# Performance work log

Measured on AMD Instinct MI355X. Metric: run time of the kernel, lower is better.

Reference implementation:

```python
import jax, jax.numpy as jnp
import numpy as np

EMBED_DIM = 1024
N_HEAD = 16
BLOCK_SIZE = 2048
B, T = 4, 2048


def setup_inputs() -> dict:
    key = jax.random.key(0)
    kx, kw, kb = jax.random.split(key, 3)
    x = jax.random.normal(kx, (B, T, EMBED_DIM), dtype=jnp.float32)
    # nn.Linear(embed_dim, 3*embed_dim): weight [3C, C], bias [3C]
    bound = 1.0 / np.sqrt(EMBED_DIM)
    W_qkv = jax.random.uniform(kw, (3 * EMBED_DIM, EMBED_DIM), dtype=jnp.float32, minval=-bound, maxval=bound)
    b_qkv = jax.random.uniform(kb, (3 * EMBED_DIM,), dtype=jnp.float32, minval=-bound, maxval=bound)
    return {"x": x, "W_qkv": W_qkv, "b_qkv": b_qkv}


def reference(x, W_qkv, b_qkv):
    Bsz, Tlen, C = x.shape
    H = N_HEAD
    hd = C // H
    qkv = x @ W_qkv.T + b_qkv  # [B, T, 3C]
    q, k, v = jnp.split(qkv, 3, axis=2)
    # [B, H, T, hd]
    q = q.reshape(Bsz, Tlen, H, hd).transpose(0, 2, 1, 3)
    k = k.reshape(Bsz, Tlen, H, hd).transpose(0, 2, 1, 3)
    v = v.reshape(Bsz, Tlen, H, hd).transpose(0, 2, 1, 3)
    att = jnp.einsum('bhqd,bhkd->bhqk', q, k) / np.sqrt(hd).astype(np.float32)
    causal = jnp.tril(jnp.ones((Tlen, Tlen), dtype=bool))
    att = jnp.where(causal[None, None, :, :], att, -jnp.inf)
    att = jax.nn.softmax(att, axis=-1)
    out = jnp.einsum('bhqk,bhkd->bhqd', att, v)  # [B, H, T, hd]
    y = out.transpose(0, 2, 1, 3).reshape(Bsz, Tlen, C)
    return y
```

## Files before the change

### kernel.cpp

```cpp
#include <hip/hip_runtime.h>


typedef unsigned short u16;
typedef short bf16x8 __attribute__((ext_vector_type(8)));
typedef float f32x4 __attribute__((ext_vector_type(4)));
typedef float f32x16 __attribute__((ext_vector_type(16)));

__device__ __forceinline__ float exp2f_hw(float x) {
  return __builtin_amdgcn_exp2f(x);
}

__device__ __forceinline__ u16 f2b(float f) {
  union { float f; unsigned u; } x; x.f = f;
  unsigned r = x.u + 0x7FFFu + ((x.u >> 16) & 1u);
  return (u16)(r >> 16);
}

__device__ __forceinline__ unsigned cvtpk(float lo, float hi_) {
  unsigned r;
  asm("v_cvt_pk_bf16_f32 %0, %1, %2" : "=v"(r) : "v"(lo), "v"(hi_));
  return r;
}

__device__ __forceinline__ void gload16(const void* g, void* l) {
  __builtin_amdgcn_global_load_lds(
      (const __attribute__((address_space(1))) unsigned*)g,
      (__attribute__((address_space(3))) unsigned*)l, 16, 0, 0);
}

__device__ __forceinline__ void packP(f32x16 st, bf16x8& pa0, bf16x8& pa1) {
#pragma unroll
  for (int r = 0; r < 16; ++r) st[r] = exp2f_hw(fminf(st[r], 80.f));
  {
    unsigned x0 = cvtpk(st[0], st[1]),  y0 = cvtpk(st[4], st[5]);
    unsigned x1 = cvtpk(st[2], st[3]),  y1 = cvtpk(st[6], st[7]);
    auto s0 = __builtin_amdgcn_permlane32_swap(x0, y0, false, false);
    auto s1 = __builtin_amdgcn_permlane32_swap(x1, y1, false, false);
    union { unsigned w[4]; bf16x8 v; } u;
    u.w[0] = s0[0]; u.w[1] = s1[0]; u.w[2] = s0[1]; u.w[3] = s1[1];
    pa0 = u.v;
  }
  {
    unsigned x0 = cvtpk(st[8], st[9]),   y0 = cvtpk(st[12], st[13]);
    unsigned x1 = cvtpk(st[10], st[11]), y1 = cvtpk(st[14], st[15]);
    auto s0 = __builtin_amdgcn_permlane32_swap(x0, y0, false, false);
    auto s1 = __builtin_amdgcn_permlane32_swap(x1, y1, false, false);
    union { unsigned w[4]; bf16x8 v; } u;
    u.w[0] = s0[0]; u.w[1] = s1[0]; u.w[2] = s0[1]; u.w[3] = s1[1];
    pa1 = u.v;
  }
}

__global__ void cvt_bf16(const float* __restrict__ src, u16* __restrict__ dst, int n4) {
  int i = blockIdx.x * blockDim.x + threadIdx.x;
  const int stride = gridDim.x * blockDim.x;
  for (; i < n4; i += stride) {
    float4 v = ((const float4*)src)[i];
    ushort4 o;
    o.x = f2b(v.x); o.y = f2b(v.y); o.z = f2b(v.z); o.w = f2b(v.w);
    ((ushort4*)dst)[i] = o;
  }
}

__global__ __launch_bounds__(256) void qkv_gemm(
    const u16* __restrict__ Xb, const u16* __restrict__ Wb,
    const float* __restrict__ bias,
    u16* __restrict__ qw, u16* __restrict__ kw, u16* __restrict__ vw) {
  __shared__ u16 LDSbuf[2][16384];
  const int tid  = threadIdx.x;
  const int lane = tid & 63;
  const int wave = tid >> 6;
  const int ln = lane & 15, hi = lane >> 4;
  const int wr = wave >> 1, wc = wave & 1;
  const int m0 = blockIdx.y * 128;
  const int n0 = blockIdx.x * 128;
  const bool vblk = (n0 >= 2048);

  const int srow = tid >> 2;
  const int scol = (tid & 3) * 8;

  f32x4 zero = {0.f, 0.f, 0.f, 0.f};
  f32x4 acc[4][4];
#pragma unroll
  for (int i = 0; i < 4; ++i)
#pragma unroll
    for (int j = 0; j < 4; ++j) acc[i][j] = zero;

  const u16* Xb0 = Xb + (size_t)(m0 + srow) * 1024 + scol;
  const u16* Xb1 = Xb + (size_t)(m0 + 64 + srow) * 1024 + scol;
  const u16* Wb0 = Wb + (size_t)(n0 + srow) * 1024 + scol;
  const u16* Wb1 = Wb + (size_t)(n0 + 64 + srow) * 1024 + scol;

  auto STAGE = [&](int cur, int k0) {
    char* As = (char*)&LDSbuf[cur][0];
    char* Bs = (char*)&LDSbuf[cur][8192];
    gload16(Xb0 + k0,      As + tid * 16);
    gload16(Xb1 + k0,      As + 4096 + tid * 16);
    gload16(Xb0 + k0 + 32, As + 8192 + tid * 16);
    gload16(Xb1 + k0 + 32, As + 12288 + tid * 16);
    gload16(Wb0 + k0,      Bs + tid * 16);
    gload16(Wb1 + k0,      Bs + 4096 + tid * 16);
    gload16(Wb0 + k0 + 32, Bs + 8192 + tid * 16);
    gload16(Wb1 + k0 + 32, Bs + 12288 + tid * 16);
  };

  auto COMPUTE = [&](int cur) {
    const u16* As = &LDSbuf[cur][0];
    const u16* Bs = &LDSbuf[cur][8192];
#pragma unroll
    for (int hf = 0; hf < 2; ++hf) {
      const u16* Ah = As + hf * 4096;
      const u16* Bh = Bs + hf * 4096;
      bf16x8 af[4], bfv[4];
#pragma unroll
      for (int i = 0; i < 4; ++i)
        af[i] = *(const bf16x8*)&Ah[(wr * 64 + i * 16 + ln) * 32 + hi * 8];
#pragma unroll
      for (int j = 0; j < 4; ++j)
        bfv[j] = *(const bf16x8*)&Bh[(wc * 64 + j * 16 + ln) * 32 + hi * 8];
      if (vblk) {
#pragma unroll
        for (int i = 0; i < 4; ++i)
#pragma unroll
          for (int j = 0; j < 4; ++j)
            acc[i][j] = __builtin_amdgcn_mfma_f32_16x16x32_bf16(bfv[j], af[i], acc[i][j], 0, 0, 0);
      } else {
#pragma unroll
        for (int i = 0; i < 4; ++i)
#pragma unroll
          for (int j = 0; j < 4; ++j)
            acc[i][j] = __builtin_amdgcn_mfma_f32_16x16x32_bf16(af[i], bfv[j], acc[i][j], 0, 0, 0);
      }
    }
  };

  STAGE(0, 0);
  __syncthreads();
  int cur = 0;
#pragma unroll 1
  for (int t = 0; t < 15; ++t) {
    STAGE(cur ^ 1, (t + 1) * 64);
    COMPUTE(cur);
    __syncthreads();
    cur ^= 1;
  }
  COMPUTE(cur);

  const int which = n0 >> 10;
  const int h = ((n0 & 1023) >> 6) + wc;
  const size_t bh = (size_t)((m0 >> 11) * 16 + h);
  const int tloc = (m0 & 2047) + wr * 64;

  if (which == 2) {
    u16* ob = vw + bh * 131072;
#pragma unroll
    for (int j = 0; j < 4; ++j) {
      float bv[4];
#pragma unroll
      for (int r = 0; r < 4; ++r) bv[r] = bias[n0 + wc * 64 + j * 16 + hi * 4 + r];
#pragma unroll
      for (int i = 0; i < 4; ++i) {
        u16* p = ob + (((tloc >> 4) + i) * 64 + j * 16 + hi * 4) * 16 + ln;
#pragma unroll
        for (int r = 0; r < 4; ++r)
          p[r * 16] = f2b(acc[i][j][r] + bv[r]);
      }
    }
  } else {
    u16* ob = (which == 0 ? qw : kw) + bh * 131072;
    const float qs = (which == 0) ? 0.1803368801111244f : 1.0f;
    const int t5 = tloc >> 5;
#pragma unroll
    for (int j = 0; j < 4; ++j) {
      const float bv = bias[n0 + wc * 64 + j * 16 + ln];
#pragma unroll
      for (int i = 0; i < 4; ++i) {
        u16* p = ob + ((t5 + (i >> 1)) * 4 + j) * 512 + ((i & 1) * 16 + hi * 4) * 16 + ln;
#pragma unroll
        for (int r = 0; r < 4; ++r)
          p[r * 16] = f2b((acc[i][j][r] + bv) * qs);
      }
    }
  }
}

__global__ __launch_bounds__(128) void attn(
    const u16* __restrict__ qw, const u16* __restrict__ kw,
    const u16* __restrict__ vw, float* __restrict__ y) {
  __shared__ float accXA[2][16][64];
  __shared__ float lXA[2][16][64];
  __shared__ float accXB[2][16][64];
  __shared__ float lXB[2][16][64];

  const int lane = threadIdx.x & 63;
  const int p    = threadIdx.x >> 6;
  const int l31 = lane & 31;
  const int hi  = lane >> 5;
  const int laneoff = l31 * 16 + hi * 8;

  const int bid = blockIdx.x;
  const int xcd = bid & 7;
  const int rest = bid >> 3;
  const int pr  = rest & 15;
  const int bh  = xcd + 8 * (rest >> 4);
  const int bb  = bh >> 4, h = bh & 15;

  const u16* qb = qw + (size_t)bh * 131072;
  const u16* kb = kw + (size_t)bh * 131072;
  const u16* vb = vw + (size_t)bh * 131072;
  float* yb = y + (size_t)bb * 2048 * 1024 + (size_t)h * 64;

  bf16x8 onesf;
#pragma unroll
  for (int j = 0; j < 8; ++j) onesf[j] = (short)0x3F80;

#pragma unroll 1
  for (int phase = 0; phase < 2; ++phase) {
    const int s  = phase ? (31 - pr) : pr;
    const int q0 = s * 64;
    const int cA = 2 * s, cB = 2 * s + 1;
    const int jtE = cB;

    bf16x8 qfA[4], qfB[4];
#pragma unroll
    for (int sb = 0; sb < 4; ++sb) {
      qfA[sb] = *(const bf16x8*)&qb[(cA * 4 + sb) * 512 + laneoff];
      qfB[sb] = *(const bf16x8*)&qb[(cB * 4 + sb) * 512 + laneoff];
    }

    f32x16 accA0, accA1, acclA, accB0, accB1, acclB;
#pragma unroll
    for (int r = 0; r < 16; ++r) {
      accA0[r] = 0.f; accA1[r] = 0.f; acclA[r] = 0.f;
      accB0[r] = 0.f; accB1[r] = 0.f; acclB[r] = 0.f;
    }

    bf16x8 kf[4];
#pragma unroll
    for (int sb = 0; sb < 4; ++sb)
      kf[sb] = *(const bf16x8*)&kb[(p * 4 + sb) * 512 + laneoff];

#pragma unroll 1
    for (int jt = p; jt <= jtE; jt += 2) {
      bf16x8 vf[4];
      vf[0] = *(const bf16x8*)&vb[((jt * 2 + 0) * 64 +  0 + l31) * 16 + hi * 8];
      vf[1] = *(const bf16x8*)&vb[((jt * 2 + 0) * 64 + 32 + l31) * 16 + hi * 8];
      vf[2] = *(const bf16x8*)&vb[((jt * 2 + 1) * 64 +  0 + l31) * 16 + hi * 8];
      vf[3] = *(const bf16x8*)&vb[((jt * 2 + 1) * 64 + 32 + l31) * 16 + hi * 8];

      f32x16 stA, stB;
#pragma unroll
      for (int r = 0; r < 16; ++r) { stA[r] = 0.f; stB[r] = 0.f; }
#pragma unroll
      for (int sb = 0; sb < 4; ++sb) {
        stA = __builtin_amdgcn_mfma_f32_32x32x16_bf16(kf[sb], qfA[sb], stA, 0, 0, 0);
        stB = __builtin_amdgcn_mfma_f32_32x32x16_bf16(kf[sb], qfB[sb], stB, 0, 0, 0);
      }
      if (jt + 2 <= jtE) {
#pragma unroll
        for (int sb = 0; sb < 4; ++sb)
          kf[sb] = *(const bf16x8*)&kb[((jt + 2) * 4 + sb) * 512 + laneoff];
      }

      if (jt == cA) {
#pragma unroll
        for (int r = 0; r < 16; ++r) {
          const int crow = (r & 3) + 8 * (r >> 2) + 4 * hi;
          if (crow > l31) stA[r] = -1e30f;
        }
      }
      if (jt == cB) {
#pragma unroll
        for (int r = 0; r < 16; ++r) {
          const int crow = (r & 3) + 8 * (r >> 2) + 4 * hi;
          stA[r] = -1e30f;
          if (crow > l31) stB[r] = -1e30f;
        }
      }

      bf16x8 pa0, pa1;
      packP(stA, pa0, pa1);
      accA0 = __builtin_amdgcn_mfma_f32_32x32x16_bf16(pa0, vf[0], accA0, 0, 0, 0);
      accA1 = __builtin_amdgcn_mfma_f32_32x32x16_bf16(pa0, vf[1], accA1, 0, 0, 0);
      acclA = __builtin_amdgcn_mfma_f32_32x32x16_bf16(pa0, onesf, acclA, 0, 0, 0);
      accA0 = __builtin_amdgcn_mfma_f32_32x32x16_bf16(pa1, vf[2], accA0, 0, 0, 0);
      accA1 = __builtin_amdgcn_mfma_f32_32x32x16_bf16(pa1, vf[3], accA1, 0, 0, 0);
      acclA = __builtin_amdgcn_mfma_f32_32x32x16_bf16(pa1, onesf, acclA, 0, 0, 0);

      packP(stB, pa0, pa1);
      accB0 = __builtin_amdgcn_mfma_f32_32x32x16_bf16(pa0, vf[0], accB0, 0, 0, 0);
      accB1 = __builtin_amdgcn_mfma_f32_32x32x16_bf16(pa0, vf[1], accB1, 0, 0, 0);
      acclB = __builtin_amdgcn_mfma_f32_32x32x16_bf16(pa0, onesf, acclB, 0, 0, 0);
      accB0 = __builtin_amdgcn_mfma_f32_32x32x16_bf16(pa1, vf[2], accB0, 0, 0, 0);
      accB1 = __builtin_amdgcn_mfma_f32_32x32x16_bf16(pa1, vf[3], accB1, 0, 0, 0);
      acclB = __builtin_amdgcn_mfma_f32_32x32x16_bf16(pa1, onesf, acclB, 0, 0, 0);
    }

    __syncthreads();
    if (p == 0) {
#pragma unroll
      for (int r = 0; r < 16; ++r) {
        accXA[0][r][lane] = accA1[r]; lXA[0][r][lane] = acclA[r];
        accXB[0][r][lane] = accB1[r]; lXB[0][r][lane] = acclB[r];
      }
    } else {
#pragma unroll
      for (int r = 0; r < 16; ++r) {
        accXA[1][r][lane] = accA0[r]; lXA[1][r][lane] = acclA[r];
        accXB[1][r][lane] = accB0[r]; lXB[1][r][lane] = acclB[r];
      }
    }
    __syncthreads();

#pragma unroll
    for (int r = 0; r < 16; ++r) {
      const int crow = (r & 3) + 8 * (r >> 2) + 4 * hi;
      const float ownA = (p == 0) ? accA0[r] : accA1[r];
      const float othA = accXA[p ^ 1][r][lane];
      const float invA = 1.0f / (acclA[r] + lXA[p ^ 1][r][lane]);
      yb[(size_t)(q0 + crow) * 1024 + p * 32 + l31] = (ownA + othA) * invA;

      const float ownB = (p == 0) ? accB0[r] : accB1[r];
      const float othB = accXB[p ^ 1][r][lane];
      const float invB = 1.0f / (acclB[r] + lXB[p ^ 1][r][lane]);
      yb[(size_t)(q0 + 32 + crow) * 1024 + p * 32 + l31] = (ownB + othB) * invB;
    }
  }
}

extern "C" void kernel_launch(void* const* d_in, const int* in_sizes, int n_in,
                              void* d_out, int out_size, void* d_ws, size_t ws_size,
                              hipStream_t stream) {
  const float* x    = (const float*)d_in[0];
  const float* W    = (const float*)d_in[1];
  const float* bias = (const float*)d_in[2];
  float* y = (float*)d_out;

  char* ws = (char*)d_ws;
  u16* xb = (u16*)(ws);
  u16* Wb = (u16*)(ws + 16777216);
  u16* qw = (u16*)(ws + 23068672);
  u16* kw = (u16*)(ws + 39845888);
  u16* vw = (u16*)(ws + 56623104);

  cvt_bf16<<<2048, 256, 0, stream>>>(x, xb, 8388608 / 4);
  cvt_bf16<<<1024, 256, 0, stream>>>(W, Wb, 3145728 / 4);
  qkv_gemm<<<dim3(24, 64), 256, 0, stream>>>(xb, Wb, bias, qw, kw, vw);
  attn<<<1024, 128, 0, stream>>>(qw, kw, vw, y);
}
```

Baseline: 134.4 us.

## Launch one attention block per query tile, heaviest tiles first

Each attention block used to process a paired light and heavy causal query tile across two phases. Now each block handles a single 64-row query tile, and the launch doubles to 2048 blocks, scheduled in descending order of work (s = 31 - ...). The shared-memory reduction buffers are halved and reused for the A and B halves in sequence. This trades the built-in load balancing of pairing for more parallelism, lower LDS use (higher occupancy), and longest-first scheduling. The cost is an extra barrier and repeated per-block setup.

```diff
diff --git a/kernel.cpp b/kernel.cpp
--- a/kernel.cpp
+++ b/kernel.cpp
@@ -187,10 +187,8 @@
 __global__ __launch_bounds__(128) void attn(
     const u16* __restrict__ qw, const u16* __restrict__ kw,
     const u16* __restrict__ vw, float* __restrict__ y) {
-  __shared__ float accXA[2][16][64];
-  __shared__ float lXA[2][16][64];
-  __shared__ float accXB[2][16][64];
-  __shared__ float lXB[2][16][64];
+  __shared__ float accX[2][16][64];
+  __shared__ float lX[2][16][64];
 
   const int lane = threadIdx.x & 63;
   const int p    = threadIdx.x >> 6;
@@ -201,8 +199,8 @@
   const int bid = blockIdx.x;
   const int xcd = bid & 7;
   const int rest = bid >> 3;
-  const int pr  = rest & 15;
-  const int bh  = xcd + 8 * (rest >> 4);
+  const int s   = 31 - (rest & 31);
+  const int bh  = xcd + 8 * (rest >> 5);
   const int bb  = bh >> 4, h = bh & 15;
 
   const u16* qb = qw + (size_t)bh * 131072;
@@ -214,117 +212,117 @@
 #pragma unroll
   for (int j = 0; j < 8; ++j) onesf[j] = (short)0x3F80;
 
+  const int q0 = s * 64;
+  const int cA = 2 * s, cB = 2 * s + 1;
+  const int jtE = cB;
+
+  bf16x8 qfA[4], qfB[4];
+#pragma unroll
+  for (int sb = 0; sb < 4; ++sb) {
+    qfA[sb] = *(const bf16x8*)&qb[(cA * 4 + sb) * 512 + laneoff];
+    qfB[sb] = *(const bf16x8*)&qb[(cB * 4 + sb) * 512 + laneoff];
+  }
+
+  f32x16 accA0, accA1, acclA, accB0, accB1, acclB;
+#pragma unroll
+  for (int r = 0; r < 16; ++r) {
+    accA0[r] = 0.f; accA1[r] = 0.f; acclA[r] = 0.f;
+    accB0[r] = 0.f; accB1[r] = 0.f; acclB[r] = 0.f;
+  }
+
+  bf16x8 kf[4];
+#pragma unroll
+  for (int sb = 0; sb < 4; ++sb)
+    kf[sb] = *(const bf16x8*)&kb[(p * 4 + sb) * 512 + laneoff];
+
 #pragma unroll 1
-  for (int phase = 0; phase < 2; ++phase) {
-    const int s  = phase ? (31 - pr) : pr;
-    const int q0 = s * 64;
-    const int cA = 2 * s, cB = 2 * s + 1;
-    const int jtE = cB;
-
-    bf16x8 qfA[4], qfB[4];
+  for (int jt = p; jt <= jtE; jt += 2) {
+    bf16x8 vf[4];
+    vf[0] = *(const bf16x8*)&vb[((jt * 2 + 0) * 64 +  0 + l31) * 16 + hi * 8];
+    vf[1] = *(const bf16x8*)&vb[((jt * 2 + 0) * 64 + 32 + l31) * 16 + hi * 8];
+    vf[2] = *(const bf16x8*)&vb[((jt * 2 + 1) * 64 +  0 + l31) * 16 + hi * 8];
+    vf[3] = *(const bf16x8*)&vb[((jt * 2 + 1) * 64 + 32 + l31) * 16 + hi * 8];
+
+    f32x16 stA, stB;
+#pragma unroll
+    for (int r = 0; r < 16; ++r) { stA[r] = 0.f; stB[r] = 0.f; }
 #pragma unroll
     for (int sb = 0; sb < 4; ++sb) {
-      qfA[sb] = *(const bf16x8*)&qb[(cA * 4 + sb) * 512 + laneoff];
-      qfB[sb] = *(const bf16x8*)&qb[(cB * 4 + sb) * 512 + laneoff];
-    }
-
-    f32x16 accA0, accA1, acclA, accB0, accB1, acclB;
-#pragma unroll
-    for (int r = 0; r < 16; ++r) {
-      accA0[r] = 0.f; accA1[r] = 0.f; acclA[r] = 0.f;
-      accB0[r] = 0.f; accB1[r] = 0.f; acclB[r] = 0.f;
-    }
-
-    bf16x8 kf[4];
-#pragma unroll
-    for (int sb = 0; sb < 4; ++sb)
-      kf[sb] = *(const bf16x8*)&kb[(p * 4 + sb) * 512 + laneoff];
-
-#pragma unroll 1
-    for (int jt = p; jt <= jtE; jt += 2) {
-      bf16x8 vf[4];
-      vf[0] = *(const bf16x8*)&vb[((jt * 2 + 0) * 64 +  0 + l31) * 16 + hi * 8];
-      vf[1] = *(const bf16x8*)&vb[((jt * 2 + 0) * 64 + 32 + l31) * 16 + hi * 8];
-      vf[2] = *(const bf16x8*)&vb[((jt * 2 + 1) * 64 +  0 + l31) * 16 + hi * 8];
-      vf[3] = *(const bf16x8*)&vb[((jt * 2 + 1) * 64 + 32 + l31) * 16 + hi * 8];
-
-      f32x16 stA, stB;
-#pragma unroll
-      for (int r = 0; r < 16; ++r) { stA[r] = 0.f; stB[r] = 0.f; }
-#pragma unroll
-      for (int sb = 0; sb < 4; ++sb) {
-        stA = __builtin_amdgcn_mfma_f32_32x32x16_bf16(kf[sb], qfA[sb], stA, 0, 0, 0);
-        stB = __builtin_amdgcn_mfma_f32_32x32x16_bf16(kf[sb], qfB[sb], stB, 0, 0, 0);
-      }
-      if (jt + 2 <= jtE) {
-#pragma unroll
-        for (int sb = 0; sb < 4; ++sb)
-          kf[sb] = *(const bf16x8*)&kb[((jt + 2) * 4 + sb) * 512 + laneoff];
-      }
-
-      if (jt == cA) {
-#pragma unroll
-        for (int r = 0; r < 16; ++r) {
-          const int crow = (r & 3) + 8 * (r >> 2) + 4 * hi;
-          if (crow > l31) stA[r] = -1e30f;
-        }
-      }
-      if (jt == cB) {
-#pragma unroll
-        for (int r = 0; r < 16; ++r) {
-          const int crow = (r & 3) + 8 * (r >> 2) + 4 * hi;
-          stA[r] = -1e30f;
-          if (crow > l31) stB[r] = -1e30f;
-        }
-      }
-
-      bf16x8 pa0, pa1;
-      packP(stA, pa0, pa1);
-      accA0 = __builtin_amdgcn_mfma_f32_32x32x16_bf16(pa0, vf[0], accA0, 0, 0, 0);
-      accA1 = __builtin_amdgcn_mfma_f32_32x32x16_bf16(pa0, vf[1], accA1, 0, 0, 0);
-      acclA = __builtin_amdgcn_mfma_f32_32x32x16_bf16(pa0, onesf, acclA, 0, 0, 0);
-      accA0 = __builtin_amdgcn_mfma_f32_32x32x16_bf16(pa1, vf[2], accA0, 0, 0, 0);
-      accA1 = __builtin_amdgcn_mfma_f32_32x32x16_bf16(pa1, vf[3], accA1, 0, 0, 0);
-      acclA = __builtin_amdgcn_mfma_f32_32x32x16_bf16(pa1, onesf, acclA, 0, 0, 0);
-
-      packP(stB, pa0, pa1);
-      accB0 = __builtin_amdgcn_mfma_f32_32x32x16_bf16(pa0, vf[0], accB0, 0, 0, 0);
-      accB1 = __builtin_amdgcn_mfma_f32_32x32x16_bf16(pa0, vf[1], accB1, 0, 0, 0);
-      acclB = __builtin_amdgcn_mfma_f32_32x32x16_bf16(pa0, onesf, acclB, 0, 0, 0);
-      accB0 = __builtin_amdgcn_mfma_f32_32x32x16_bf16(pa1, vf[2], accB0, 0, 0, 0);
-      accB1 = __builtin_amdgcn_mfma_f32_32x32x16_bf16(pa1, vf[3], accB1, 0, 0, 0);
-      acclB = __builtin_amdgcn_mfma_f32_32x32x16_bf16(pa1, onesf, acclB, 0, 0, 0);
-    }
-
-    __syncthreads();
-    if (p == 0) {
+      stA = __builtin_amdgcn_mfma_f32_32x32x16_bf16(kf[sb], qfA[sb], stA, 0, 0, 0);
+      stB = __builtin_amdgcn_mfma_f32_32x32x16_bf16(kf[sb], qfB[sb], stB, 0, 0, 0);
+    }
+    if (jt + 2 <= jtE) {
+#pragma unroll
+      for (int sb = 0; sb < 4; ++sb)
+        kf[sb] = *(const bf16x8*)&kb[((jt + 2) * 4 + sb) * 512 + laneoff];
+    }
+
+    if (jt == cA) {
 #pragma unroll
       for (int r = 0; r < 16; ++r) {
-        accXA[0][r][lane] = accA1[r]; lXA[0][r][lane] = acclA[r];
-        accXB[0][r][lane] = accB1[r]; lXB[0][r][lane] = acclB[r];
-      }
-    } else {
+        const int crow = (r & 3) + 8 * (r >> 2) + 4 * hi;
+        if (crow > l31) stA[r] = -1e30f;
+      }
+    }
+    if (jt == cB) {
 #pragma unroll
       for (int r = 0; r < 16; ++r) {
-        accXA[1][r][lane] = accA0[r]; lXA[1][r][lane] = acclA[r];
-        accXB[1][r][lane] = accB0[r]; lXB[1][r][lane] = acclB[r];
-      }
-    }
-    __syncthreads();
-
-#pragma unroll
-    for (int r = 0; r < 16; ++r) {
-      const int crow = (r & 3) + 8 * (r >> 2) + 4 * hi;
-      const float ownA = (p == 0) ? accA0[r] : accA1[r];
-      const float othA = accXA[p ^ 1][r][lane];
-      const float invA = 1.0f / (acclA[r] + lXA[p ^ 1][r][lane]);
-      yb[(size_t)(q0 + crow) * 1024 + p * 32 + l31] = (ownA + othA) * invA;
-
-      const float ownB = (p == 0) ? accB0[r] : accB1[r];
-      const float othB = accXB[p ^ 1][r][lane];
-      const float invB = 1.0f / (acclB[r] + lXB[p ^ 1][r][lane]);
-      yb[(size_t)(q0 + 32 + crow) * 1024 + p * 32 + l31] = (ownB + othB) * invB;
-    }
+        const int crow = (r & 3) + 8 * (r >> 2) + 4 * hi;
+        stA[r] = -1e30f;
+        if (crow > l31) stB[r] = -1e30f;
+      }
+    }
+
+    bf16x8 pa0, pa1;
+    packP(stA, pa0, pa1);
+    accA0 = __builtin_amdgcn_mfma_f32_32x32x16_bf16(pa0, vf[0], accA0, 0, 0, 0);
+    accA1 = __builtin_amdgcn_mfma_f32_32x32x16_bf16(pa0, vf[1], accA1, 0, 0, 0);
+    acclA = __builtin_amdgcn_mfma_f32_32x32x16_bf16(pa0, onesf, acclA, 0, 0, 0);
+    accA0 = __builtin_amdgcn_mfma_f32_32x32x16_bf16(pa1, vf[2], accA0, 0, 0, 0);
+    accA1 = __builtin_amdgcn_mfma_f32_32x32x16_bf16(pa1, vf[3], accA1, 0, 0, 0);
+    acclA = __builtin_amdgcn_mfma_f32_32x32x16_bf16(pa1, onesf, acclA, 0, 0, 0);
+
+    packP(stB, pa0, pa1);
+    accB0 = __builtin_amdgcn_mfma_f32_32x32x16_bf16(pa0, vf[0], accB0, 0, 0, 0);
+    accB1 = __builtin_amdgcn_mfma_f32_32x32x16_bf16(pa0, vf[1], accB1, 0, 0, 0);
+    acclB = __builtin_amdgcn_mfma_f32_32x32x16_bf16(pa0, onesf, acclB, 0, 0, 0);
+    accB0 = __builtin_amdgcn_mfma_f32_32x32x16_bf16(pa1, vf[2], accB0, 0, 0, 0);
+    accB1 = __builtin_amdgcn_mfma_f32_32x32x16_bf16(pa1, vf[3], accB1, 0, 0, 0);
+    acclB = __builtin_amdgcn_mfma_f32_32x32x16_bf16(pa1, onesf, acclB, 0, 0, 0);
+  }
+
+  if (p == 0) {
+#pragma unroll
+    for (int r = 0; r < 16; ++r) { accX[0][r][lane] = accA1[r]; lX[0][r][lane] = acclA[r]; }
+  } else {
+#pragma unroll
+    for (int r = 0; r < 16; ++r) { accX[1][r][lane] = accA0[r]; lX[1][r][lane] = acclA[r]; }
+  }
+  __syncthreads();
+#pragma unroll
+  for (int r = 0; r < 16; ++r) {
+    const int crow = (r & 3) + 8 * (r >> 2) + 4 * hi;
+    const float own = (p == 0) ? accA0[r] : accA1[r];
+    const float oth = accX[p ^ 1][r][lane];
+    const float inv = 1.0f / (acclA[r] + lX[p ^ 1][r][lane]);
+    yb[(size_t)(q0 + crow) * 1024 + p * 32 + l31] = (own + oth) * inv;
+  }
+  __syncthreads();
+  if (p == 0) {
+#pragma unroll
+    for (int r = 0; r < 16; ++r) { accX[0][r][lane] = accB1[r]; lX[0][r][lane] = acclB[r]; }
+  } else {
+#pragma unroll
+    for (int r = 0; r < 16; ++r) { accX[1][r][lane] = accB0[r]; lX[1][r][lane] = acclB[r]; }
+  }
+  __syncthreads();
+#pragma unroll
+  for (int r = 0; r < 16; ++r) {
+    const int crow = (r & 3) + 8 * (r >> 2) + 4 * hi;
+    const float own = (p == 0) ? accB0[r] : accB1[r];
+    const float oth = accX[p ^ 1][r][lane];
+    const float inv = 1.0f / (acclB[r] + lX[p ^ 1][r][lane]);
+    yb[(size_t)(q0 + 32 + crow) * 1024 + p * 32 + l31] = (own + oth) * inv;
   }
 }
 
@@ -346,5 +344,5 @@
   cvt_bf16<<<2048, 256, 0, stream>>>(x, xb, 8388608 / 4);
   cvt_bf16<<<1024, 256, 0, stream>>>(W, Wb, 3145728 / 4);
   qkv_gemm<<<dim3(24, 64), 256, 0, stream>>>(xb, Wb, bias, qw, kw, vw);
-  attn<<<1024, 128, 0, stream>>>(qw, kw, vw, y);
-}
+  attn<<<2048, 128, 0, stream>>>(qw, kw, vw, y);
+}
```

Result: slower. 153.6 us (+14.3%).
